# Kernel tuning notes

Hardware: AMD Instinct MI355X
Metric: run time of the kernel (lower is better)

The kernel has to match this reference:

```python
import jax, jax.numpy as jnp
import numpy as np

N = 5000        # n_stocks (nodes)
F = 128         # n_features
H = 4           # attention heads
C = 32          # hidden_size per head
HC = H * C      # GAT output dim = GRU input dim
GH = 256        # gru_hidden_size
E = 320000      # directed edges (before self-loops)
NEG_SLOPE = 0.2 # GATv2Conv default leaky_relu slope


def setup_inputs() -> dict:
    key = jax.random.key(0)
    ks = jax.random.split(key, 16)
    s = 0.05
    return {
        "x": jax.random.normal(ks[0], (N, F), dtype=jnp.float32),
        "edge_index": jax.random.randint(ks[1], (2, E), 0, N, dtype=jnp.int64),
        # GATv2Conv params (lin_l, lin_r with bias, attention vector, output bias)
        "W_l": jax.random.normal(ks[2], (F, HC), dtype=jnp.float32) * s,
        "b_l": jax.random.normal(ks[3], (HC,), dtype=jnp.float32) * s,
        "W_r": jax.random.normal(ks[4], (F, HC), dtype=jnp.float32) * s,
        "b_r": jax.random.normal(ks[5], (HC,), dtype=jnp.float32) * s,
        "att": jax.random.normal(ks[6], (H, C), dtype=jnp.float32) * s,
        "gat_bias": jax.random.normal(ks[7], (HC,), dtype=jnp.float32) * s,
        # GRU params (single layer, PyTorch gate order r,z,n)
        "W_ih": jax.random.normal(ks[8], (3 * GH, HC), dtype=jnp.float32) * s,
        "W_hh": jax.random.normal(ks[9], (3 * GH, GH), dtype=jnp.float32) * s,
        "b_ih": jax.random.normal(ks[10], (3 * GH,), dtype=jnp.float32) * s,
        "b_hh": jax.random.normal(ks[11], (3 * GH,), dtype=jnp.float32) * s,
        # policy head + log_std param
        "Wp": jax.random.normal(ks[12], (N, GH), dtype=jnp.float32) * s,
        "bp": jax.random.normal(ks[13], (N,), dtype=jnp.float32) * s,
        "log_std": jnp.zeros((N,), dtype=jnp.float32),
    }


def reference(x, edge_index, W_l, b_l, W_r, b_r, att, gat_bias,
              W_ih, W_hh, b_ih, b_hh, Wp, bp, log_std):
    # --- GATv2Conv (add_self_loops=True, concat heads, eval mode -> no dropout) ---
    loop = jnp.arange(N, dtype=edge_index.dtype)
    src = jnp.concatenate([edge_index[0], loop])  # message source j
    dst = jnp.concatenate([edge_index[1], loop])  # message target i

    xl = (x @ W_l + b_l).reshape(N, H, C)  # source-side transform
    xr = (x @ W_r + b_r).reshape(N, H, C)  # target-side transform

    m = xl[src] + xr[dst]                                  # [Etot, H, C]
    e = jnp.einsum('ehc,hc->eh', jax.nn.leaky_relu(m, NEG_SLOPE), att)

    # segment softmax over incoming edges per target node
    emax = jax.ops.segment_max(e, dst, num_segments=N)      # [N, H]
    ex = jnp.exp(e - emax[dst])
    denom = jax.ops.segment_sum(ex, dst, num_segments=N)    # [N, H]
    alpha = ex / denom[dst]                                 # [Etot, H]

    agg = jax.ops.segment_sum(alpha[:, :, None] * xl[src], dst, num_segments=N)
    gat_out = agg.reshape(N, HC) + gat_bias                 # [N, H*C]

    # --- GRU: each node = one batch element, seq_len=1, h0 = 0 ---
    gi = gat_out @ W_ih.T + b_ih                            # [N, 3*GH]
    gr, gz, gn = jnp.split(gi, 3, axis=1)
    hr, hz, hn = jnp.split(b_hh, 3)                          # h0=0 -> only hh bias
    r = jax.nn.sigmoid(gr + hr)
    z = jax.nn.sigmoid(gz + hz)
    n = jnp.tanh(gn + r * hn)
    h = (1.0 - z) * n                                        # [N, GH]

    # --- policy head ---
    mean = h @ Wp.T + bp                                     # [N, N]
    std = jnp.exp(jnp.clip(log_std, -10.0, 2.0))             # [N]
    return mean, std
```

## Files before the change

kernel.cpp:

```cpp
#include <hip/hip_runtime.h>
#include <hip/hip_bf16.h>
#include <float.h>

#define N_NODES 5000
#define F_IN    128
#define HC      128
#define GH      256
#define NE      320000
#define NET     325000
#define MPAD    5120
#define CAP     160
#define LIN_BLKS   313
#define DEC_BLKS  1270
#define NTHR    (DEC_BLKS * 256)

typedef __bf16 bf16;
typedef __attribute__((ext_vector_type(4))) __bf16 bf16x4;
typedef __attribute__((ext_vector_type(8))) __bf16 bf16x8;
typedef __attribute__((ext_vector_type(4))) float  f32x4;

__device__ __forceinline__ float lrelu(float v) { return v > 0.f ? v : 0.2f * v; }
__device__ __forceinline__ float sigm(float v) { return 1.f / (1.f + __expf(-v)); }

__device__ __forceinline__ void gload16(const void* g, void* l) {
  __builtin_amdgcn_global_load_lds((const __attribute__((address_space(1))) void*)g,
                                   (__attribute__((address_space(3))) void*)l, 16, 0, 0);
}

__global__ void k_init(int* __restrict__ cnt) {
  int i = blockIdx.x * 256 + threadIdx.x;
  if (i < N_NODES) cnt[i] = 0;
}

#define NWIH (768 * HC)
#define NWP  (N_NODES * GH)
__global__ __launch_bounds__(256) void k_pre(
    const float* __restrict__ x,
    const float* __restrict__ Wl, const float* __restrict__ bl,
    const float* __restrict__ Wr, const float* __restrict__ br,
    bf16* __restrict__ xlb, bf16* __restrict__ xrb,
    const float* __restrict__ lstd, float* __restrict__ out_std,
    const int* __restrict__ ei, int* __restrict__ cnt, int* __restrict__ csr_s,
    const float* __restrict__ wih, const float* __restrict__ wp,
    bf16* __restrict__ wihb, bf16* __restrict__ wpb) {
  __shared__ float xs[16][F_IN];
  int t = threadIdx.x;
  if (blockIdx.x < LIN_BLKS) {
    int nb = blockIdx.x * 16;
#pragma unroll
    for (int p = 0; p < 8; ++p) {
      int idx = p * 256 + t;
      int nl = idx >> 7, c = idx & 127;
      int gn = nb + nl;
      xs[nl][c] = (gn < N_NODES) ? x[(size_t)gn * F_IN + c] : 0.f;
    }
    __syncthreads();
    int col = t & 127;
    const float* W = (t < 128) ? Wl : Wr;
    float bias = (t < 128) ? bl[col] : br[col];
    float acc[16];
#pragma unroll
    for (int m = 0; m < 16; ++m) acc[m] = bias;
#pragma unroll 4
    for (int k = 0; k < F_IN; ++k) {
      float w = W[k * HC + col];
#pragma unroll
      for (int m = 0; m < 16; ++m) acc[m] = fmaf(xs[m][k], w, acc[m]);
    }
    bf16* out = (t < 128) ? xlb : xrb;
#pragma unroll
    for (int m = 0; m < 16; ++m) {
      int gn = nb + m;
      if (gn < N_NODES) out[(size_t)gn * HC + col] = (bf16)acc[m];
    }
    if (t < 16) {
      int gn = nb + t;
      if (gn < N_NODES) out_std[gn] = expf(fminf(fmaxf(lstd[gn], -10.f), 2.f));
    }
    return;
  }
  __shared__ int mode;
  if (t == 0) {
    int f = 0;
    for (int q = 1; q < 128; q += 2) f |= ei[q];
    mode = (f == 0) ? 1 : 0;
  }
  __syncthreads();
  int e = (blockIdx.x - LIN_BLKS) * 256 + t;
  for (int i = e; i < NWIH / 4; i += NTHR) {
    float4 v = reinterpret_cast<const float4*>(wih)[i];
    bf16x4 o = {(bf16)v.x, (bf16)v.y, (bf16)v.z, (bf16)v.w};
    *reinterpret_cast<bf16x4*>(&wihb[i * 4]) = o;
  }
  for (int i = e; i < NWP / 4; i += NTHR) {
    float4 v = reinterpret_cast<const float4*>(wp)[i];
    bf16x4 o = {(bf16)v.x, (bf16)v.y, (bf16)v.z, (bf16)v.w};
    *reinterpret_cast<bf16x4*>(&wpb[i * 4]) = o;
  }
  if (e >= NET) return;
  int s, d;
  if (e >= NE) { s = d = e - NE; }
  else if (mode) { s = ei[2 * e]; d = ei[2 * (NE + e)]; }
  else           { s = ei[e];     d = ei[NE + e]; }
  int slot = atomicAdd(&cnt[d], 1);
  if (slot < CAP) csr_s[d * CAP + slot] = s;
}

__global__ __launch_bounds__(256) void k_gat(
    const bf16* __restrict__ xlb, const bf16* __restrict__ xrb,
    const int* __restrict__ csr_s, const int* __restrict__ cnt,
    const float* __restrict__ att, const float* __restrict__ gbias,
    bf16* __restrict__ gat_b) {
  int t = threadIdx.x;
  int lane = t & 63;
  int node = blockIdx.x * 4 + (t >> 6);
  if (node >= N_NODES) return;
  int c8 = lane & 15;
  int eg = lane >> 4;
  bf16x8 xr8 = *reinterpret_cast<const bf16x8*>(xrb + (size_t)node * HC + c8 * 8);
  float4 w0 = reinterpret_cast<const float4*>(att)[c8 * 2];
  float4 w1 = reinterpret_cast<const float4*>(att)[c8 * 2 + 1];
  float xr[8], wv[8];
#pragma unroll
  for (int k = 0; k < 8; ++k) xr[k] = (float)xr8[k];
  wv[0] = w0.x; wv[1] = w0.y; wv[2] = w0.z; wv[3] = w0.w;
  wv[4] = w1.x; wv[5] = w1.y; wv[6] = w1.z; wv[7] = w1.w;

  float acc[8] = {0.f, 0.f, 0.f, 0.f, 0.f, 0.f, 0.f, 0.f};
  float den = 0.f;
  int deg = cnt[node];
  deg = deg < CAP ? deg : CAP;
  int beg = node * CAP, end = node * CAP + deg;
#pragma unroll 2
  for (int p0 = beg; p0 < end; p0 += 4) {
    int p = p0 + eg;
    bool valid = p < end;
    int j = valid ? csr_s[p] : node;
    bf16x8 a8 = *reinterpret_cast<const bf16x8*>(xlb + (size_t)j * HC + c8 * 8);
    float av[8];
    float tt = 0.f;
#pragma unroll
    for (int k = 0; k < 8; ++k) {
      av[k] = (float)a8[k];
      tt = fmaf(lrelu(av[k] + xr[k]), wv[k], tt);
    }
    tt += __shfl_xor(tt, 1);
    tt += __shfl_xor(tt, 2);
    float pe = valid ? __expf(tt) : 0.f;
    den += pe;
#pragma unroll
    for (int k = 0; k < 8; ++k) acc[k] = fmaf(pe, av[k], acc[k]);
  }
#pragma unroll
  for (int m = 16; m <= 32; m <<= 1) {
    den += __shfl_xor(den, m);
#pragma unroll
    for (int k = 0; k < 8; ++k) acc[k] += __shfl_xor(acc[k], m);
  }
  if (eg == 0) {
    float4 g0 = reinterpret_cast<const float4*>(gbias)[c8 * 2];
    float4 g1 = reinterpret_cast<const float4*>(gbias)[c8 * 2 + 1];
    float gb[8] = {g0.x, g0.y, g0.z, g0.w, g1.x, g1.y, g1.z, g1.w};
    float rden = 1.f / den;
    bf16x8 o;
#pragma unroll
    for (int k = 0; k < 8; ++k) o[k] = (bf16)(acc[k] * rden + gb[k]);
    *reinterpret_cast<bf16x8*>(gat_b + (size_t)node * HC + c8 * 8) = o;
  }
}

__global__ __launch_bounds__(256) void k_gemm_gru(
    const bf16* __restrict__ A, const bf16* __restrict__ wihb,
    const float* __restrict__ bih, const float* __restrict__ bhh,
    bf16* __restrict__ hb) {
  __shared__ char smem[49152];
  char* Ab = smem;
  char* Bb = smem + 16384;
  int t = threadIdx.x;
  int lane = t & 63, wave = t >> 6;
  int wm = wave >> 1, wn = wave & 1;
  int r16 = lane & 15, kg = lane >> 4;
  int sw7 = r16 & 7;
  int bm = blockIdx.x >> 1, bn = blockIdx.x & 1;
  int r0 = bm * 64, c0 = bn * 128;

#pragma unroll
  for (int q = 0; q < 4; ++q) {
    int idx = q * 256 + t;
    int half = idx >> 9, ih = idx & 511;
    int row = ih >> 3, cc = ih & 7;
    int gc = cc ^ (row & 7);
    gload16(&A[(size_t)(r0 + row) * 128 + half * 64 + gc * 8],
            Ab + (q * 256 + wave * 64) * 16);
  }

  auto STAGE_B = [&](int gate) {
#pragma unroll
    for (int q = 0; q < 8; ++q) {
      int idx = q * 256 + t;
      int half = idx >> 10, ih = idx & 1023;
      int row = ih >> 3, cc = ih & 7;
      int gc = cc ^ (row & 7);
      gload16(&wihb[(size_t)(gate * 256 + c0 + row) * 128 + half * 64 + gc * 8],
              Bb + (q * 256 + wave * 64) * 16);
    }
  };

  int rowA[2], rowB[4];
#pragma unroll
  for (int m = 0; m < 2; ++m) rowA[m] = (wm * 32 + m * 16 + r16) * 128;
#pragma unroll
  for (int n = 0; n < 4; ++n) rowB[n] = (wn * 64 + n * 16 + r16) * 128;

  f32x4 acc[3][2][4] = {};
  STAGE_B(0);
  __syncthreads();
#pragma unroll
  for (int g = 0; g < 3; ++g) {
#pragma unroll
    for (int h = 0; h < 2; ++h)
#pragma unroll
      for (int w = 0; w < 2; ++w) {
        int ch = ((w * 4 + kg) ^ sw7) * 16;
        bf16x8 af[2], bfr[4];
#pragma unroll
        for (int m = 0; m < 2; ++m)
          af[m] = *reinterpret_cast<const bf16x8*>(Ab + h * 8192 + rowA[m] + ch);
#pragma unroll
        for (int n = 0; n < 4; ++n)
          bfr[n] = *reinterpret_cast<const bf16x8*>(Bb + h * 16384 + rowB[n] + ch);
#pragma unroll
        for (int m = 0; m < 2; ++m)
#pragma unroll
          for (int n = 0; n < 4; ++n)
            acc[g][m][n] = __builtin_amdgcn_mfma_f32_16x16x32_bf16(af[m], bfr[n], acc[g][m][n], 0, 0, 0);
      }
    __syncthreads();
    if (g < 2) { STAGE_B(g + 1); __syncthreads(); }
  }

  bf16* hl = (bf16*)Bb;
#pragma unroll
  for (int n = 0; n < 4; ++n) {
    int c = c0 + wn * 64 + n * 16 + r16;
    float bihr = bih[c],      bhhr = bhh[c];
    float bihz = bih[256 + c], bhhz = bhh[256 + c];
    float bihn = bih[512 + c], bhhn = bhh[512 + c];
#pragma unroll
    for (int m = 0; m < 2; ++m)
#pragma unroll
      for (int rr = 0; rr < 4; ++rr) {
        float rg = sigm(acc[0][m][n][rr] + bihr + bhhr);
        float zg = sigm(acc[1][m][n][rr] + bihz + bhhz);
        float ng = tanhf(acc[2][m][n][rr] + bihn + rg * bhhn);
        float hv = (1.f - zg) * ng;
        int row = wm * 32 + m * 16 + kg * 4 + rr;
        hl[row * 128 + (wn * 64 + n * 16 + r16)] = (bf16)hv;
      }
  }
  __syncthreads();
#pragma unroll
  for (int q = 0; q < 4; ++q) {
    int idx = q * 256 + t;
    int row = idx >> 4, cc = idx & 15;
    int node = r0 + row;
    if (node < N_NODES + 120)
      *reinterpret_cast<int4*>(&hb[(size_t)node * GH + c0 + cc * 8]) =
          *reinterpret_cast<const int4*>(&hl[row * 128 + cc * 8]);
  }
}

__global__ __launch_bounds__(256) void gemm_nt_f32out(
    const bf16* __restrict__ A, const bf16* __restrict__ B,
    const float* __restrict__ bias, float* __restrict__ Cout,
    int K, int ldc, int Mstore, int Nstore, int nbx) {
  __shared__ char smem[65536];
  int t = threadIdx.x;
  int lane = t & 63, wave = t >> 6;
  int wm = wave >> 1, wn = wave & 1;
  int r16 = lane & 15, kg = lane >> 4;

  int nwg = gridDim.x;
  int cpx = nwg >> 3;
  int wg  = blockIdx.x;
  int swz = (wg & 7) * cpx + (wg >> 3);
  int bm0 = (swz % nbx) * 128;
  int bn0 = (swz / nbx) * 128;

  int rsub = lane >> 3;
  int cchk = lane & 7;

  auto STAGE = [&](int buf, int k0) {
    char* Ab = smem + buf * 32768;
#pragma unroll
    for (int q = 0; q < 4; ++q) {
      int row = (wave * 4 + q) * 8 + rsub;
      int gc = cchk ^ (row & 7);
      char* db = Ab + (wave * 4 + q) * 1024;
      gload16(&A[(size_t)(bm0 + row) * K + k0 + gc * 8], db);
      gload16(&B[(size_t)(bn0 + row) * K + k0 + gc * 8], db + 16384);
    }
  };

  f32x4 acc[4][4] = {};
  int rbA[4], rbB[4];
#pragma unroll
  for (int m = 0; m < 4; ++m) rbA[m] = (wm * 64 + m * 16 + r16) * 128;
#pragma unroll
  for (int n = 0; n < 4; ++n) rbB[n] = (wn * 64 + n * 16 + r16) * 128;
  int sw7 = r16 & 7;

  int nt = K >> 6;
  STAGE(0, 0);
  __syncthreads();
  for (int tt = 0; tt < nt; ++tt) {
    if (tt + 1 < nt) STAGE((tt & 1) ^ 1, (tt + 1) * 64);
    const char* Ab = smem + (tt & 1) * 32768;
    const char* Bb = Ab + 16384;
#pragma unroll
    for (int ks = 0; ks < 2; ++ks) {
      int ch = ((ks * 4 + kg) ^ sw7) * 16;
      bf16x8 af[4], bfr[4];
#pragma unroll
      for (int m = 0; m < 4; ++m)
        af[m] = *reinterpret_cast<const bf16x8*>(Ab + rbA[m] + ch);
#pragma unroll
      for (int n = 0; n < 4; ++n)
        bfr[n] = *reinterpret_cast<const bf16x8*>(Bb + rbB[n] + ch);
#pragma unroll
      for (int m = 0; m < 4; ++m)
#pragma unroll
        for (int n = 0; n < 4; ++n)
          acc[m][n] = __builtin_amdgcn_mfma_f32_16x16x32_bf16(af[m], bfr[n], acc[m][n], 0, 0, 0);
    }
    __syncthreads();
  }

  float bv[4];
#pragma unroll
  for (int n = 0; n < 4; ++n) {
    int gcol = bn0 + wn * 64 + n * 16 + r16;
    bv[n] = (gcol < Nstore) ? bias[gcol] : 0.f;
  }

  float* Cs = (float*)smem;
#pragma unroll
  for (int m = 0; m < 4; ++m) {
    int rb = wm * 64 + m * 16 + kg * 4;
#pragma unroll
    for (int n = 0; n < 4; ++n) {
      int cb = wn * 64 + n * 16 + r16;
#pragma unroll
      for (int r = 0; r < 4; ++r)
        Cs[(rb + r) * 128 + cb] = acc[m][n][r] + bv[n];
    }
  }
  __syncthreads();
#pragma unroll
  for (int i = 0; i < 16; ++i) {
    int chunk = i * 256 + t;
    int row = chunk >> 5, cc = chunk & 31;
    int grow = bm0 + row, gcol = bn0 + cc * 4;
    if (grow < Mstore && gcol < Nstore) {
      f32x4 v = *reinterpret_cast<const f32x4*>(&Cs[row * 128 + cc * 4]);
      __builtin_nontemporal_store(v, reinterpret_cast<f32x4*>(&Cout[(size_t)grow * ldc + gcol]));
    }
  }
}

extern "C" void kernel_launch(void* const* d_in, const int* in_sizes, int n_in,
                              void* d_out, int out_size, void* d_ws, size_t ws_size,
                              hipStream_t stream) {
  const float* x     = (const float*)d_in[0];
  const int*   ei    = (const int*)d_in[1];
  const float* Wl    = (const float*)d_in[2];
  const float* bl    = (const float*)d_in[3];
  const float* Wr    = (const float*)d_in[4];
  const float* br    = (const float*)d_in[5];
  const float* att   = (const float*)d_in[6];
  const float* gbias = (const float*)d_in[7];
  const float* Wih   = (const float*)d_in[8];
  const float* bih   = (const float*)d_in[10];
  const float* bhh   = (const float*)d_in[11];
  const float* Wp    = (const float*)d_in[12];
  const float* bp    = (const float*)d_in[13];
  const float* lstd  = (const float*)d_in[14];
  float* out_mean = (float*)d_out;
  float* out_std  = out_mean + (size_t)N_NODES * N_NODES;

  char* w = (char*)d_ws;
  auto carve = [&](size_t bytes) {
    char* p = w; w += (bytes + 255) & ~(size_t)255; return p;
  };
  bf16*  xlb   = (bf16*)carve((size_t)N_NODES * HC * 2);
  bf16*  xrb   = (bf16*)carve((size_t)N_NODES * HC * 2);
  int*   cnt   = (int*)carve((size_t)N_NODES * 4);
  int*   csr_s = (int*)carve((size_t)N_NODES * CAP * 4);
  bf16*  gatb  = (bf16*)carve((size_t)MPAD * HC * 2);
  bf16*  wihb  = (bf16*)carve((size_t)768 * HC * 2);
  bf16*  hb    = (bf16*)carve((size_t)MPAD * GH * 2);
  bf16*  wpb   = (bf16*)carve((size_t)MPAD * GH * 2);

  k_init<<<(N_NODES + 255) / 256, 256, 0, stream>>>(cnt);
  k_pre<<<LIN_BLKS + DEC_BLKS, 256, 0, stream>>>(
      x, Wl, bl, Wr, br, xlb, xrb, lstd, out_std,
      ei, cnt, csr_s, Wih, Wp, wihb, wpb);
  k_gat<<<(N_NODES + 3) / 4, 256, 0, stream>>>(xlb, xrb, csr_s, cnt, att, gbias, gatb);
  k_gemm_gru<<<160, 256, 0, stream>>>(gatb, wihb, bih, bhh, hb);
  gemm_nt_f32out<<<40 * 40, 256, 0, stream>>>(hb, wpb, bp, out_mean, 256, N_NODES, N_NODES, N_NODES, 40);
}
```

Baseline: 112.6 us.

## Halve GRU GEMM row tile, double-buffer weight stages, vectorize edge loads

The GRU input GEMM kernel now uses 32-row tiles instead of 64, launching 320 blocks rather than 160 to fill more compute units. It also double-buffers the per-gate weight tiles in a larger LDS allocation, so the next gate's load overlaps the current gate's MFMAs and one barrier per gate is dropped. Separately, the int64 edge-index path reads each index as an int2 vector load. The trade-off is that each block reloads the same weight tiles for less work and needs 72KB of LDS, which may lower occupancy. The row guard on the store was removed, which relies on the padded buffer.

Result: no change. 110.6 us (-1.8%).

```diff
diff --git a/kernel.cpp b/kernel.cpp
--- a/kernel.cpp
+++ b/kernel.cpp
@@ -100,8 +100,11 @@
   if (e >= NET) return;
   int s, d;
   if (e >= NE) { s = d = e - NE; }
-  else if (mode) { s = ei[2 * e]; d = ei[2 * (NE + e)]; }
-  else           { s = ei[e];     d = ei[NE + e]; }
+  else if (mode) {
+    int2 sv = *reinterpret_cast<const int2*>(&ei[2 * e]);
+    int2 dv = *reinterpret_cast<const int2*>(&ei[2 * (NE + e)]);
+    s = sv.x; d = dv.x;
+  } else { s = ei[e]; d = ei[NE + e]; }
   int slot = atomicAdd(&cnt[d], 1);
   if (slot < CAP) csr_s[d * CAP + slot] = s;
 }
@@ -173,28 +176,28 @@
     const bf16* __restrict__ A, const bf16* __restrict__ wihb,
     const float* __restrict__ bih, const float* __restrict__ bhh,
     bf16* __restrict__ hb) {
-  __shared__ char smem[49152];
+  __shared__ char smem[73728];
   char* Ab = smem;
-  char* Bb = smem + 16384;
   int t = threadIdx.x;
   int lane = t & 63, wave = t >> 6;
   int wm = wave >> 1, wn = wave & 1;
   int r16 = lane & 15, kg = lane >> 4;
   int sw7 = r16 & 7;
   int bm = blockIdx.x >> 1, bn = blockIdx.x & 1;
-  int r0 = bm * 64, c0 = bn * 128;
-
-#pragma unroll
-  for (int q = 0; q < 4; ++q) {
+  int r0 = bm * 32, c0 = bn * 128;
+
+#pragma unroll
+  for (int q = 0; q < 2; ++q) {
     int idx = q * 256 + t;
-    int half = idx >> 9, ih = idx & 511;
+    int half = idx >> 8, ih = idx & 255;
     int row = ih >> 3, cc = ih & 7;
     int gc = cc ^ (row & 7);
     gload16(&A[(size_t)(r0 + row) * 128 + half * 64 + gc * 8],
             Ab + (q * 256 + wave * 64) * 16);
   }
 
-  auto STAGE_B = [&](int gate) {
+  auto STAGE_B = [&](int gate, int buf) {
+    char* Bb = smem + 8192 + buf * 32768;
 #pragma unroll
     for (int q = 0; q < 8; ++q) {
       int idx = q * 256 + t;
@@ -206,67 +209,59 @@
     }
   };
 
-  int rowA[2], rowB[4];
-#pragma unroll
-  for (int m = 0; m < 2; ++m) rowA[m] = (wm * 32 + m * 16 + r16) * 128;
+  int rowA = (wm * 16 + r16) * 128;
+  int rowB[4];
 #pragma unroll
   for (int n = 0; n < 4; ++n) rowB[n] = (wn * 64 + n * 16 + r16) * 128;
 
-  f32x4 acc[3][2][4] = {};
-  STAGE_B(0);
+  f32x4 acc[3][4] = {};
+  STAGE_B(0, 0);
   __syncthreads();
 #pragma unroll
   for (int g = 0; g < 3; ++g) {
+    if (g < 2) STAGE_B(g + 1, (g + 1) & 1);
+    const char* Bb = smem + 8192 + (g & 1) * 32768;
 #pragma unroll
     for (int h = 0; h < 2; ++h)
 #pragma unroll
       for (int w = 0; w < 2; ++w) {
         int ch = ((w * 4 + kg) ^ sw7) * 16;
-        bf16x8 af[2], bfr[4];
-#pragma unroll
-        for (int m = 0; m < 2; ++m)
-          af[m] = *reinterpret_cast<const bf16x8*>(Ab + h * 8192 + rowA[m] + ch);
+        bf16x8 af = *reinterpret_cast<const bf16x8*>(Ab + h * 4096 + rowA + ch);
+        bf16x8 bfr[4];
 #pragma unroll
         for (int n = 0; n < 4; ++n)
           bfr[n] = *reinterpret_cast<const bf16x8*>(Bb + h * 16384 + rowB[n] + ch);
 #pragma unroll
-        for (int m = 0; m < 2; ++m)
-#pragma unroll
-          for (int n = 0; n < 4; ++n)
-            acc[g][m][n] = __builtin_amdgcn_mfma_f32_16x16x32_bf16(af[m], bfr[n], acc[g][m][n], 0, 0, 0);
+        for (int n = 0; n < 4; ++n)
+          acc[g][n] = __builtin_amdgcn_mfma_f32_16x16x32_bf16(af, bfr[n], acc[g][n], 0, 0, 0);
       }
     __syncthreads();
-    if (g < 2) { STAGE_B(g + 1); __syncthreads(); }
-  }
-
-  bf16* hl = (bf16*)Bb;
+  }
+
+  bf16* hl = (bf16*)Ab;
 #pragma unroll
   for (int n = 0; n < 4; ++n) {
     int c = c0 + wn * 64 + n * 16 + r16;
-    float bihr = bih[c],      bhhr = bhh[c];
+    float bihr = bih[c],       bhhr = bhh[c];
     float bihz = bih[256 + c], bhhz = bhh[256 + c];
     float bihn = bih[512 + c], bhhn = bhh[512 + c];
 #pragma unroll
-    for (int m = 0; m < 2; ++m)
-#pragma unroll
-      for (int rr = 0; rr < 4; ++rr) {
-        float rg = sigm(acc[0][m][n][rr] + bihr + bhhr);
-        float zg = sigm(acc[1][m][n][rr] + bihz + bhhz);
-        float ng = tanhf(acc[2][m][n][rr] + bihn + rg * bhhn);
-        float hv = (1.f - zg) * ng;
-        int row = wm * 32 + m * 16 + kg * 4 + rr;
-        hl[row * 128 + (wn * 64 + n * 16 + r16)] = (bf16)hv;
-      }
+    for (int rr = 0; rr < 4; ++rr) {
+      float rg = sigm(acc[0][n][rr] + bihr + bhhr);
+      float zg = sigm(acc[1][n][rr] + bihz + bhhz);
+      float ng = tanhf(acc[2][n][rr] + bihn + rg * bhhn);
+      float hv = (1.f - zg) * ng;
+      int row = wm * 16 + kg * 4 + rr;
+      hl[row * 128 + (wn * 64 + n * 16 + r16)] = (bf16)hv;
+    }
   }
   __syncthreads();
 #pragma unroll
-  for (int q = 0; q < 4; ++q) {
+  for (int q = 0; q < 2; ++q) {
     int idx = q * 256 + t;
     int row = idx >> 4, cc = idx & 15;
-    int node = r0 + row;
-    if (node < N_NODES + 120)
-      *reinterpret_cast<int4*>(&hb[(size_t)node * GH + c0 + cc * 8]) =
-          *reinterpret_cast<const int4*>(&hl[row * 128 + cc * 8]);
+    *reinterpret_cast<int4*>(&hb[(size_t)(r0 + row) * GH + c0 + cc * 8]) =
+        *reinterpret_cast<const int4*>(&hl[row * 128 + cc * 8]);
   }
 }
 
@@ -406,6 +401,6 @@
       x, Wl, bl, Wr, br, xlb, xrb, lstd, out_std,
       ei, cnt, csr_s, Wih, Wp, wihb, wpb);
   k_gat<<<(N_NODES + 3) / 4, 256, 0, stream>>>(xlb, xrb, csr_s, cnt, att, gbias, gatb);
-  k_gemm_gru<<<160, 256, 0, stream>>>(gatb, wihb, bih, bhh, hb);
+  k_gemm_gru<<<320, 256, 0, stream>>>(gatb, wihb, bih, bhh, hb);
   gemm_nt_f32out<<<40 * 40, 256, 0, stream>>>(hb, wpb, bp, out_mean, 256, N_NODES, N_NODES, N_NODES, 40);
 }
```
